# Kernel optimization log

Hardware: AMD Instinct MI355X
Metric: run time of the kernel (lower is better)

The kernel has to match this reference:

```python
import jax, jax.numpy as jnp
import numpy as np

B, N, E = 128, 300, 300        # batch, nodes (max_length), edges per sample
DIN, DH, DOUT = 768, 256, 256  # input feat, gcn hidden, gcn output
R = 26                         # NUM_DEP_TYPES
NHEADS, HDIM = 8, DH // 8


def setup_inputs() -> dict:
    key = jax.random.key(0)
    ks = jax.random.split(key, 12)
    s = lambda d: 1.0 / np.sqrt(d)
    return {
        "node_features": jax.random.normal(ks[0], (B, N, DIN), jnp.float32),
        "src": jax.random.randint(ks[1], (B, E), 0, N, jnp.int32),
        "dst": jax.random.randint(ks[2], (B, E), 0, N, jnp.int32),
        "etype": jax.random.randint(ks[3], (B, E), 0, R, jnp.int32),
        "W_rel": jax.random.normal(ks[4], (R, DIN, DH), jnp.float32) * s(DIN),
        "W_loop": jax.random.normal(ks[5], (DIN, DH), jnp.float32) * s(DIN),
        "b_rel": jnp.zeros((DH,), jnp.float32),
        "in_proj_w": jax.random.normal(ks[6], (3 * DH, DH), jnp.float32) * s(DH),
        "in_proj_b": jnp.zeros((3 * DH,), jnp.float32),
        "out_proj_w": jax.random.normal(ks[7], (DH, DH), jnp.float32) * s(DH),
        "out_proj_b": jnp.zeros((DH,), jnp.float32),
        "mlp_w": jax.random.normal(ks[8], (DOUT, DH), jnp.float32) * s(DH),
        "mlp_b": jnp.zeros((DOUT,), jnp.float32),
    }


def reference(node_features, src, dst, etype, W_rel, W_loop, b_rel,
              in_proj_w, in_proj_b, out_proj_w, out_proj_b, mlp_w, mlp_b):
    # ---- RelGraphConv (regularizer=None, self_loop=True, sum aggregation) ----
    # gather source-node features per edge: [B, E, DIN]
    h_src = jnp.take_along_axis(node_features, src[..., None].astype(jnp.int32), axis=1)
    # per-relation masked matmul: msg[b,e] = h_src[b,e] @ W_rel[etype[b,e]]
    msg = jnp.zeros((B, E, DH), node_features.dtype)
    for r in range(R):  # fixed small relation set
        mask = (etype == r)[..., None]
        msg = msg + jnp.einsum('bei,io->beo', jnp.where(mask, h_src, 0.0), W_rel[r])
    # scatter-add messages to destination nodes
    b_idx = jnp.arange(B)[:, None]
    agg = jnp.zeros((B, N, DH), node_features.dtype).at[b_idx, dst].add(msg)
    h = agg + jnp.einsum('bni,io->bno', node_features, W_loop) + b_rel  # [B, N, DH]

    # ---- MultiheadAttention (self-attn over nodes, eval mode) ----
    qkv = jnp.einsum('bnd,ed->bne', h, in_proj_w) + in_proj_b
    q, k, v = jnp.split(qkv, 3, axis=-1)
    q = q.reshape(B, N, NHEADS, HDIM)
    k = k.reshape(B, N, NHEADS, HDIM)
    v = v.reshape(B, N, NHEADS, HDIM)
    scores = jnp.einsum('bqhd,bkhd->bhqk', q, k) / np.sqrt(HDIM)
    attn = jax.nn.softmax(scores, axis=-1)
    ctx = jnp.einsum('bhqk,bkhd->bqhd', attn, v).reshape(B, N, DH)
    attn_out = jnp.einsum('bnd,ed->bne', ctx, out_proj_w) + out_proj_b

    # ---- mean-pool over nodes + MLP ----
    pooled = jnp.mean(attn_out, axis=1)  # [B, DH]
    return pooled @ mlp_w.T + mlp_b      # [B, DOUT]
```

## Files before the change

### kernel.cpp

```cpp
#include <hip/hip_runtime.h>
#include <hip/hip_bf16.h>
#include <cstdint>
#include <cstddef>

#define BB 128
#define NN 300
#define EE 300
#define DIN 768
#define DH 256
#define NREL 26
#define NHEADS 8
#define HDIM 32
#define MTOT (BB*NN)
#define NEDGE (BB*EE)
#define NHB 150

typedef __attribute__((ext_vector_type(8))) short bf16x8;
typedef __attribute__((ext_vector_type(4))) float f32x4;
typedef unsigned short u16;
union BU { uint4 u; bf16x8 v; };

__device__ __forceinline__ unsigned int packbf2(float a, float b) {
    unsigned int ua = __float_as_uint(a);
    unsigned int ub = __float_as_uint(b);
    ua = (ua + 0x7FFFu + ((ua >> 16) & 1u)) >> 16;
    ub = (ub + 0x7FFFu + ((ub >> 16) & 1u)) & 0xFFFF0000u;
    return ua | ub;
}
__device__ __forceinline__ u16 packbf1(float a) {
    unsigned int ua = __float_as_uint(a);
    return (u16)((ua + 0x7FFFu + ((ua >> 16) & 1u)) >> 16);
}
__device__ __forceinline__ unsigned cvtpk(float a, float b) {
    union { __hip_bfloat162 h; unsigned u; } cv;
    cv.h = __float22bfloat162_rn(make_float2(a, b));
    return cv.u;
}

__global__ __launch_bounds__(256) void b_hist(const int* __restrict__ etype,
                                              int* __restrict__ blockhist) {
    __shared__ int hist[NREL];
    const int tid = threadIdx.x;
    if (tid < NREL) hist[tid] = 0;
    __syncthreads();
    atomicAdd(&hist[etype[blockIdx.x * 256 + tid]], 1);
    __syncthreads();
    if (tid < NREL) blockhist[blockIdx.x * NREL + tid] = hist[tid];
}

__global__ __launch_bounds__(64) void b_scan(const int* __restrict__ blockhist,
                                             int* __restrict__ blockbase,
                                             int* __restrict__ cnt, int* __restrict__ off) {
    __shared__ int tot[NREL];
    const int r = threadIdx.x;
    if (r < NREL) {
        int run = 0;
        for (int b = 0; b < NHB; ++b) {
            blockbase[b * NREL + r] = run;
            run += blockhist[b * NREL + r];
        }
        tot[r] = run;
        cnt[r] = run;
    }
    __syncthreads();
    __shared__ int offs[NREL + 1];
    if (r == 0) {
        int acc = 0;
        for (int q = 0; q < NREL; ++q) { offs[q] = acc; off[q] = acc; acc += tot[q]; }
        offs[NREL] = acc; off[NREL] = acc;
    }
    __syncthreads();
    if (r < NREL) {
        int o = offs[r];
        for (int b = 0; b < NHB; ++b) blockbase[b * NREL + r] += o;
    }
}

__global__ __launch_bounds__(256) void b_scatter(const int* __restrict__ etype,
                                                 const int* __restrict__ blockbase,
                                                 int* __restrict__ list) {
    __shared__ int wavehist[4][NREL];
    __shared__ int waveoff[4][NREL];
    const int tid = threadIdx.x;
    const int w = tid >> 6, l = tid & 63;
    const int i = blockIdx.x * 256 + tid;
    const int r = etype[i];
    unsigned long long mymask = 0ull;
    #pragma unroll
    for (int q = 0; q < NREL; ++q) {
        unsigned long long m = __ballot(r == q);
        if (l == 0) wavehist[w][q] = __popcll(m);
        if (r == q) mymask = m;
    }
    const int myrank = __popcll(mymask & ((1ull << l) - 1ull));
    __syncthreads();
    if (tid < NREL) {
        int acc = 0;
        #pragma unroll
        for (int ww = 0; ww < 4; ++ww) { waveoff[ww][tid] = acc; acc += wavehist[ww][tid]; }
    }
    __syncthreads();
    list[blockbase[blockIdx.x * NREL + r] + waveoff[w][r] + myrank] = i;
}

__global__ __launch_bounds__(128) void z_tail(uint4* __restrict__ vg4) {
    const int p = blockIdx.x;
    const int tid = threadIdx.x;
    const int f = (tid < 64) ? 9 : 19;
    const int t = tid & 63;
    vg4[(size_t)(p * 20 + f) * 64 + t] = make_uint4(0u, 0u, 0u, 0u);
}

__global__ __launch_bounds__(256) void c_cast8(const float4* __restrict__ in,
                                               uint4* __restrict__ out, int n8) {
    int i = blockIdx.x * 256 + threadIdx.x;
    if (i < n8) {
        float4 f0 = in[2*i], f1 = in[2*i+1];
        uint4 o;
        o.x = packbf2(f0.x, f0.y); o.y = packbf2(f0.z, f0.w);
        o.z = packbf2(f1.x, f1.y); o.w = packbf2(f1.z, f1.w);
        out[i] = o;
    }
}

__global__ __launch_bounds__(256) void c_cast_w(
    const float* __restrict__ wrel, const float* __restrict__ wl, const float* __restrict__ wq,
    uint4* __restrict__ wrb, uint4* __restrict__ wlb, uint4* __restrict__ wqb) {
    int t = blockIdx.x * 256 + threadIdx.x;
    int l = t & 63, fid = t >> 6;
    if (fid < NREL*24*16) {
        int r = fid / 384, rem = fid - r * 384;
        int kf = rem >> 4, nt = rem & 15;
        int k0 = 32*kf + 8*(l >> 4), n = 16*nt + (l & 15);
        const float* p = wrel + ((size_t)r*768 + k0) * 256 + n;
        uint4 o;
        o.x = packbf2(p[0], p[256]); o.y = packbf2(p[512], p[768]);
        o.z = packbf2(p[1024], p[1280]); o.w = packbf2(p[1536], p[1792]);
        wrb[t] = o;
    } else if (fid < NREL*24*16 + 384) {
        int f2 = fid - NREL*24*16;
        int kf = f2 >> 4, nt = f2 & 15;
        int k0 = 32*kf + 8*(l >> 4), n = 16*nt + (l & 15);
        const float* p = wl + (size_t)k0 * 256 + n;
        uint4 o;
        o.x = packbf2(p[0], p[256]); o.y = packbf2(p[512], p[768]);
        o.z = packbf2(p[1024], p[1280]); o.w = packbf2(p[1536], p[1792]);
        wlb[f2*64 + l] = o;
    } else {
        int f2 = fid - NREL*24*16 - 384;
        int kf = f2 / 48, nt = f2 % 48;
        int e = 16*nt + (l & 15), d0 = 32*kf + 8*(l >> 4);
        const float4* p = (const float4*)(wq + (size_t)e * 256 + d0);
        float4 f0 = p[0], f1 = p[1];
        uint4 o;
        o.x = packbf2(f0.x, f0.y); o.y = packbf2(f0.z, f0.w);
        o.z = packbf2(f1.x, f1.y); o.w = packbf2(f1.z, f1.w);
        wqb[f2*64 + l] = o;
    }
}

__global__ __launch_bounds__(256) void k1m(
    const uint4* __restrict__ xb, const uint4* __restrict__ wlb,
    const float* __restrict__ brel, float* __restrict__ h) {
    __shared__ uint4 As[1024];
    const int tid = threadIdx.x;
    const int m0 = blockIdx.x * 128;
    const int nb = blockIdx.y;
    const int w = tid >> 6, l = tid & 63;
    const int g = l >> 4, q = l & 15;
    int cA[4];
    #pragma unroll
    for (int p = 0; p < 4; ++p) {
        int s = tid + p * 256;
        int fi = s >> 6, l2 = s & 63;
        int kf = fi >> 3, mt = fi & 7;
        int row = m0 + 16*mt + (l2 & 15);
        cA[p] = row * 96 + 4*kf + (l2 >> 4);
    }
    f32x4 acc[8][2];
    #pragma unroll
    for (int a = 0; a < 8; ++a)
        #pragma unroll
        for (int n = 0; n < 2; ++n) acc[a][n] = (f32x4){0.f,0.f,0.f,0.f};

    for (int step = 0; step < 12; ++step) {
        uint4 a0 = xb[cA[0] + step*8];
        uint4 a1 = xb[cA[1] + step*8];
        uint4 a2 = xb[cA[2] + step*8];
        uint4 a3 = xb[cA[3] + step*8];
        BU Bf[2][2];
        #pragma unroll
        for (int kf = 0; kf < 2; ++kf)
            #pragma unroll
            for (int nt = 0; nt < 2; ++nt)
                Bf[kf][nt].u = wlb[((step*2 + kf)*16 + nb*8 + w*2 + nt)*64 + l];
        __syncthreads();
        As[tid] = a0; As[tid + 256] = a1; As[tid + 512] = a2; As[tid + 768] = a3;
        __syncthreads();
        #pragma unroll
        for (int kf = 0; kf < 2; ++kf) {
            #pragma unroll
            for (int mt = 0; mt < 8; ++mt) {
                BU Af; Af.u = As[(kf*8 + mt)*64 + l];
                #pragma unroll
                for (int nt = 0; nt < 2; ++nt)
                    acc[mt][nt] = __builtin_amdgcn_mfma_f32_16x16x32_bf16(Af.v, Bf[kf][nt].v, acc[mt][nt], 0, 0, 0);
            }
        }
    }
    #pragma unroll
    for (int nt = 0; nt < 2; ++nt) {
        int col = nb*128 + w*32 + nt*16 + q;
        float bias = brel[col];
        #pragma unroll
        for (int mt = 0; mt < 8; ++mt)
            #pragma unroll
            for (int i = 0; i < 4; ++i)
                h[(size_t)(m0 + 16*mt + 4*g + i)*256 + col] = acc[mt][nt][i] + bias;
    }
}

__global__ __launch_bounds__(256) void k2m(
    const uint4* __restrict__ xb, const uint4* __restrict__ wrb,
    const int* __restrict__ src, const int* __restrict__ dst,
    const int* __restrict__ cnt, const int* __restrict__ off,
    const int* __restrict__ list, float* __restrict__ h) {
    __shared__ uint4 As[1024];
    __shared__ int arow_s[128];
    __shared__ int drow_s[128];
    const int r = blockIdx.y;
    const int c_total = cnt[r];
    const int t0 = blockIdx.x * 128;
    if (t0 >= c_total) return;
    const int nb = blockIdx.z;
    const int tid = threadIdx.x;
    if (tid < 128) {
        int e = t0 + tid;
        int ar = 0, dr = -1;
        if (e < c_total) {
            int eid = list[off[r] + e];
            int b = eid / EE;
            ar = b * NN + src[eid];
            dr = b * NN + dst[eid];
        }
        arow_s[tid] = ar; drow_s[tid] = dr;
    }
    __syncthreads();
    const int w = tid >> 6, l = tid & 63;
    const int g = l >> 4, q = l & 15;
    int cA[4];
    #pragma unroll
    for (int p = 0; p < 4; ++p) {
        int s = tid + p * 256;
        int fi = s >> 6, l2 = s & 63;
        int kf = fi >> 3, mt = fi & 7;
        int row = arow_s[16*mt + (l2 & 15)];
        cA[p] = row * 96 + 4*kf + (l2 >> 4);
    }
    const uint4* wb = wrb + (size_t)r * 24*16*64;
    f32x4 acc[8][2];
    #pragma unroll
    for (int a = 0; a < 8; ++a)
        #pragma unroll
        for (int n = 0; n < 2; ++n) acc[a][n] = (f32x4){0.f,0.f,0.f,0.f};

    for (int step = 0; step < 12; ++step) {
        uint4 a0 = xb[cA[0] + step*8];
        uint4 a1 = xb[cA[1] + step*8];
        uint4 a2 = xb[cA[2] + step*8];
        uint4 a3 = xb[cA[3] + step*8];
        BU Bf[2][2];
        #pragma unroll
        for (int kf = 0; kf < 2; ++kf)
            #pragma unroll
            for (int nt = 0; nt < 2; ++nt)
                Bf[kf][nt].u = wb[((step*2 + kf)*16 + nb*8 + w*2 + nt)*64 + l];
        __syncthreads();
        As[tid] = a0; As[tid + 256] = a1; As[tid + 512] = a2; As[tid + 768] = a3;
        __syncthreads();
        #pragma unroll
        for (int kf = 0; kf < 2; ++kf) {
            #pragma unroll
            for (int mt = 0; mt < 8; ++mt) {
                BU Af; Af.u = As[(kf*8 + mt)*64 + l];
                #pragma unroll
                for (int nt = 0; nt < 2; ++nt)
                    acc[mt][nt] = __builtin_amdgcn_mfma_f32_16x16x32_bf16(Af.v, Bf[kf][nt].v, acc[mt][nt], 0, 0, 0);
            }
        }
    }
    #pragma unroll
    for (int mt = 0; mt < 8; ++mt)
        #pragma unroll
        for (int i = 0; i < 4; ++i) {
            int dr = drow_s[16*mt + 4*g + i];
            if (dr >= 0) {
                #pragma unroll
                for (int nt = 0; nt < 2; ++nt)
                    atomicAdd(&h[(size_t)dr*256 + nb*128 + w*32 + nt*16 + q], acc[mt][nt][i]);
            }
        }
}

__global__ __launch_bounds__(256) void k3m(
    const float* __restrict__ h, const uint4* __restrict__ wqb,
    const float* __restrict__ bq,
    u16* __restrict__ qg, u16* __restrict__ kg, u16* __restrict__ vg) {
    __shared__ uint4 Aall[2048];
    const int tid = threadIdx.x;
    const int m0 = blockIdx.x * 64;
    const int w = tid >> 6, l = tid & 63;
    const int g = l >> 4, q = l & 15;

    #pragma unroll
    for (int p = 0; p < 8; ++p) {
        int s = tid + p * 256;
        int fi = s >> 6, l2 = s & 63;
        int kf = fi >> 2, mt = fi & 3;
        int row = m0 + 16*mt + (l2 & 15);
        int k0 = 32*kf + 8*(l2 >> 4);
        const float4* hp = (const float4*)(h + (size_t)row * 256 + k0);
        float4 f0 = hp[0], f1 = hp[1];
        uint4 o;
        o.x = packbf2(f0.x, f0.y); o.y = packbf2(f0.z, f0.w);
        o.z = packbf2(f1.x, f1.y); o.w = packbf2(f1.z, f1.w);
        Aall[s] = o;
    }
    __syncthreads();

    for (int nb = 0; nb < 6; ++nb) {
        f32x4 acc[4][2];
        #pragma unroll
        for (int a = 0; a < 4; ++a)
            #pragma unroll
            for (int n = 0; n < 2; ++n) acc[a][n] = (f32x4){0.f,0.f,0.f,0.f};

        #pragma unroll
        for (int step = 0; step < 4; ++step) {
            BU Bf[2][2];
            #pragma unroll
            for (int kf = 0; kf < 2; ++kf)
                #pragma unroll
                for (int nt = 0; nt < 2; ++nt)
                    Bf[kf][nt].u = wqb[((step*2 + kf)*48 + nb*8 + w*2 + nt)*64 + l];
            #pragma unroll
            for (int kf = 0; kf < 2; ++kf) {
                #pragma unroll
                for (int mt = 0; mt < 4; ++mt) {
                    BU Af; Af.u = Aall[((step*2 + kf)*4 + mt)*64 + l];
                    #pragma unroll
                    for (int nt = 0; nt < 2; ++nt)
                        acc[mt][nt] = __builtin_amdgcn_mfma_f32_16x16x32_bf16(Af.v, Bf[kf][nt].v, acc[mt][nt], 0, 0, 0);
                }
            }
        }
        #pragma unroll
        for (int nt = 0; nt < 2; ++nt) {
            int e = nb*128 + w*32 + nt*16 + q;
            float bias = bq[e];
            int region = e >> 8;
            int hh = (e & 255) >> 5;
            int d  = e & 31;
            u16* outb = (region == 0) ? qg : (region == 1) ? kg : vg;
            #pragma unroll
            for (int mt = 0; mt < 4; ++mt) {
                #pragma unroll
                for (int i = 0; i < 4; ++i) {
                    int j = m0 + 16*mt + 4*g + i;
                    int b_ = j / 300;
                    int jn = j - b_ * 300;
                    u16 val = packbf1(acc[mt][nt][i] + bias);
                    size_t byte;
                    if (region < 2) {
                        int word = ((b_*8 + hh)*19 + (jn >> 4))*64 + 16*(d >> 3) + (jn & 15);
                        byte = (size_t)word*16 + (size_t)(d & 7)*2;
                    } else {
                        int word = ((b_*8 + hh)*20 + (d >> 4)*10 + (jn >> 5))*64 + 16*((jn >> 3) & 3) + (d & 15);
                        byte = (size_t)word*16 + (size_t)(jn & 7)*2;
                    }
                    *(u16*)((char*)outb + byte) = val;
                }
            }
        }
    }
}

__global__ __launch_bounds__(256) void k4_attn(
    const uint4* __restrict__ qg, const uint4* __restrict__ kg,
    const uint4* __restrict__ vg, float* __restrict__ pooled) {
    __shared__ uint4 kf_s[19*64];
    __shared__ uint4 vt_s[20*64];
    __shared__ __align__(16) u16 pbuf[4][2560];
    __shared__ float pool_lds[4][32];
    const int bh = blockIdx.x;
    const int tid = threadIdx.x;
    for (int s = tid; s < 19*64; s += 256) kf_s[s] = kg[(size_t)bh*19*64 + s];
    for (int s = tid; s < 20*64; s += 256) vt_s[s] = vg[(size_t)bh*20*64 + s];
    __syncthreads();

    const int w = tid >> 6, l = tid & 63;
    const int g = l >> 4, q = l & 15;
    char* pwbase = (char*)pbuf[w] + 256*(g >> 1) + 16*q + 8*(g & 1);
    const uint4* prd = (const uint4*)pbuf[w];

    const float c1 = 0.17677669529663687f * 1.4426950408889634f;
    float pool[8] = {0.f,0.f,0.f,0.f,0.f,0.f,0.f,0.f};

    for (int qt = w; qt < 19; qt += 4) {
        const int qrow = qt * 16 + q;
        BU uq; uq.u = qg[(size_t)(bh*19 + qt)*64 + l];
        float lsum = 0.f;
        f32x4 ctx0 = {0.f,0.f,0.f,0.f}, ctx1 = {0.f,0.f,0.f,0.f};

        #pragma unroll
        for (int half = 0; half < 2; ++half) {
            #pragma unroll
            for (int jj = 0; jj < 10; ++jj) {
                const int jt = half*10 + jj;
                uint2 pk = make_uint2(0u, 0u);
                if (jt < 19) {
                    BU uk; uk.u = kf_s[jt*64 + l];
                    f32x4 z = {0.f,0.f,0.f,0.f};
                    f32x4 s4 = __builtin_amdgcn_mfma_f32_16x16x32_bf16(uk.v, uq.v, z, 0, 0, 0);
                    float p0 = exp2f(s4[0]*c1);
                    float p1 = exp2f(s4[1]*c1);
                    float p2 = exp2f(s4[2]*c1);
                    float p3 = exp2f(s4[3]*c1);
                    if (jt == 18 && g == 3) { p0 = 0.f; p1 = 0.f; p2 = 0.f; p3 = 0.f; }
                    lsum += (p0 + p1) + (p2 + p3);
                    pk.x = cvtpk(p0, p1);
                    pk.y = cvtpk(p2, p3);
                }
                *(uint2*)(pwbase + 512*jj) = pk;
            }
            #pragma unroll
            for (int cc = 0; cc < 5; ++cc) {
                const int cg = half*5 + cc;
                BU up;  up.u  = prd[cc*64 + l];
                BU uv0; uv0.u = vt_s[cg*64 + l];
                BU uv1; uv1.u = vt_s[(10 + cg)*64 + l];
                ctx0 = __builtin_amdgcn_mfma_f32_16x16x32_bf16(uv0.v, up.v, ctx0, 0, 0, 0);
                ctx1 = __builtin_amdgcn_mfma_f32_16x16x32_bf16(uv1.v, up.v, ctx1, 0, 0, 0);
            }
        }
        lsum += __shfl_xor(lsum, 16);
        lsum += __shfl_xor(lsum, 32);
        if (qrow < NN) {
            float inv = 1.0f / lsum;
            pool[0] += ctx0[0] * inv; pool[1] += ctx0[1] * inv;
            pool[2] += ctx0[2] * inv; pool[3] += ctx0[3] * inv;
            pool[4] += ctx1[0] * inv; pool[5] += ctx1[1] * inv;
            pool[6] += ctx1[2] * inv; pool[7] += ctx1[3] * inv;
        }
    }

    #pragma unroll
    for (int i = 0; i < 8; ++i) {
        float v = pool[i];
        v += __shfl_xor(v, 1); v += __shfl_xor(v, 2);
        v += __shfl_xor(v, 4); v += __shfl_xor(v, 8);
        pool[i] = v;
    }
    if (q == 0) {
        #pragma unroll
        for (int dt = 0; dt < 2; ++dt)
            #pragma unroll
            for (int i = 0; i < 4; ++i)
                pool_lds[w][dt * 16 + 4 * g + i] = pool[dt * 4 + i];
    }
    __syncthreads();
    if (tid < 32) {
        int b = bh >> 3, hh = bh & 7;
        float s = pool_lds[0][tid] + pool_lds[1][tid] + pool_lds[2][tid] + pool_lds[3][tid];
        pooled[(size_t)b * DH + hh * HDIM + tid] = s * (1.0f / 300.0f);
    }
}

__global__ __launch_bounds__(256) void k5_head(
    const float* __restrict__ pooled, const float* __restrict__ wo, const float* __restrict__ bo,
    const float* __restrict__ wm, const float* __restrict__ bm, float* __restrict__ out) {
    __shared__ float pc[DH];
    __shared__ float t1[DH];
    const int b = blockIdx.x, tid = threadIdx.x;
    pc[tid] = pooled[(size_t)b * DH + tid];
    __syncthreads();
    float acc = bo[tid];
    for (int d = 0; d < DH; ++d) acc += pc[d] * wo[(size_t)tid * DH + d];
    t1[tid] = acc;
    __syncthreads();
    float acc2 = bm[tid];
    for (int e2 = 0; e2 < DH; ++e2) acc2 += t1[e2] * wm[(size_t)tid * DH + e2];
    out[(size_t)b * DH + tid] = acc2;
}

extern "C" void kernel_launch(void* const* d_in, const int* in_sizes, int n_in,
                              void* d_out, int out_size, void* d_ws, size_t ws_size,
                              hipStream_t stream) {
    (void)in_sizes; (void)n_in; (void)out_size; (void)ws_size;
    const float* x     = (const float*)d_in[0];
    const int*   src   = (const int*)d_in[1];
    const int*   dst   = (const int*)d_in[2];
    const int*   etype = (const int*)d_in[3];
    const float* wrel  = (const float*)d_in[4];
    const float* wloop = (const float*)d_in[5];
    const float* brel  = (const float*)d_in[6];
    const float* wq    = (const float*)d_in[7];
    const float* bq    = (const float*)d_in[8];
    const float* wo    = (const float*)d_in[9];
    const float* bo    = (const float*)d_in[10];
    const float* wm    = (const float*)d_in[11];
    const float* bm    = (const float*)d_in[12];
    float* out = (float*)d_out;

    char* W = (char*)d_ws;
    float* h      = (float*)W;
    u16*   vg     = (u16*)W;
    u16*   xb     = (u16*)(W + 39321600ull);
    u16*   qg     = xb;
    u16*   kg     = (u16*)(W + 39321600ull + 19922944ull);
    u16*   hb_dead= (u16*)(W + 39321600ull + 58982400ull);
    uint4* wrb    = (uint4*)(W + 39321600ull + 58982400ull + 19660800ull);
    uint4* wlb    = (uint4*)((char*)wrb + 10223616ull);
    uint4* wqb    = (uint4*)((char*)wlb + 393216ull);
    float* pooled = (float*)((char*)wqb + 393216ull);
    int*   ibase  = (int*)((char*)pooled + 131072ull);
    int*   cnt    = ibase;
    int*   off    = ibase + 32;
    int*   list   = ibase + 64;
    int*   blockhist = list + NEDGE;
    int*   blockbase = blockhist + NHB*NREL;
    (void)hb_dead;

    vg = (u16*)((char*)(blockbase + NHB*NREL) + 256);
    vg = (u16*)(((uintptr_t)vg + 255) & ~(uintptr_t)255);

    b_hist<<<NHB, 256, 0, stream>>>(etype, blockhist);
    b_scan<<<1, 64, 0, stream>>>(blockhist, blockbase, cnt, off);
    b_scatter<<<NHB, 256, 0, stream>>>(etype, blockbase, list);

    c_cast8<<<14400, 256, 0, stream>>>((const float4*)x, (uint4*)xb, 3686400);
    c_cast_w<<<2688, 256, 0, stream>>>(wrel, wloop, wq, wrb, wlb, wqb);

    k1m<<<dim3(300, 2), 256, 0, stream>>>((const uint4*)xb, wlb, brel, h);
    k2m<<<dim3(16, 26, 2), 256, 0, stream>>>((const uint4*)xb, wrb, src, dst, cnt, off, list, h);
    z_tail<<<1024, 128, 0, stream>>>((uint4*)vg);
    k3m<<<600, 256, 0, stream>>>(h, wqb, bq, qg, kg, vg);
    k4_attn<<<BB * NHEADS, 256, 0, stream>>>((const uint4*)qg, (const uint4*)kg, (const uint4*)vg, pooled);
    k5_head<<<BB, 256, 0, stream>>>(pooled, wo, bo, wm, bm, out);
}
```

Measured before the change: 285.0 us.

## Pre-cast h to bf16 and split QKV projection across output blocks in grid

Adds a separate cast kernel that converts the fp32 GCN output h to bf16 once. The QKV projection kernel now launches one block per (64-row tile, 128-column output block), giving 3600 blocks instead of 600, and streams the bf16 A tile through a small LDS buffer per k-step instead of staging the full 64x256 tile. This raises parallelism and lowers LDS use per block. The cost is an extra kernel launch and an extra pass over h, and each A tile is now read six times from global memory or cache.

```diff
diff --git a/kernel.cpp b/kernel.cpp
--- a/kernel.cpp
+++ b/kernel.cpp
@@ -303,83 +303,79 @@
 }
 
 __global__ __launch_bounds__(256) void k3m(
-    const float* __restrict__ h, const uint4* __restrict__ wqb,
+    const uint4* __restrict__ hb, const uint4* __restrict__ wqb,
     const float* __restrict__ bq,
     u16* __restrict__ qg, u16* __restrict__ kg, u16* __restrict__ vg) {
-    __shared__ uint4 Aall[2048];
+    __shared__ uint4 As[512];
     const int tid = threadIdx.x;
     const int m0 = blockIdx.x * 64;
+    const int nb = blockIdx.y;
     const int w = tid >> 6, l = tid & 63;
     const int g = l >> 4, q = l & 15;
-
-    #pragma unroll
-    for (int p = 0; p < 8; ++p) {
+    int cA[2];
+    #pragma unroll
+    for (int p = 0; p < 2; ++p) {
         int s = tid + p * 256;
         int fi = s >> 6, l2 = s & 63;
         int kf = fi >> 2, mt = fi & 3;
         int row = m0 + 16*mt + (l2 & 15);
-        int k0 = 32*kf + 8*(l2 >> 4);
-        const float4* hp = (const float4*)(h + (size_t)row * 256 + k0);
-        float4 f0 = hp[0], f1 = hp[1];
-        uint4 o;
-        o.x = packbf2(f0.x, f0.y); o.y = packbf2(f0.z, f0.w);
-        o.z = packbf2(f1.x, f1.y); o.w = packbf2(f1.z, f1.w);
-        Aall[s] = o;
-    }
-    __syncthreads();
-
-    for (int nb = 0; nb < 6; ++nb) {
-        f32x4 acc[4][2];
-        #pragma unroll
-        for (int a = 0; a < 4; ++a)
-            #pragma unroll
-            for (int n = 0; n < 2; ++n) acc[a][n] = (f32x4){0.f,0.f,0.f,0.f};
-
-        #pragma unroll
-        for (int step = 0; step < 4; ++step) {
-            BU Bf[2][2];
-            #pragma unroll
-            for (int kf = 0; kf < 2; ++kf)
+        cA[p] = row * 32 + 4*kf + (l2 >> 4);
+    }
+    f32x4 acc[4][2];
+    #pragma unroll
+    for (int a = 0; a < 4; ++a)
+        #pragma unroll
+        for (int n = 0; n < 2; ++n) acc[a][n] = (f32x4){0.f,0.f,0.f,0.f};
+
+    for (int step = 0; step < 4; ++step) {
+        uint4 a0 = hb[cA[0] + step*8];
+        uint4 a1 = hb[cA[1] + step*8];
+        BU Bf[2][2];
+        #pragma unroll
+        for (int kf = 0; kf < 2; ++kf)
+            #pragma unroll
+            for (int nt = 0; nt < 2; ++nt)
+                Bf[kf][nt].u = wqb[((step*2 + kf)*48 + nb*8 + w*2 + nt)*64 + l];
+        __syncthreads();
+        As[tid] = a0; As[tid + 256] = a1;
+        __syncthreads();
+        #pragma unroll
+        for (int kf = 0; kf < 2; ++kf) {
+            BU Af[4];
+            #pragma unroll
+            for (int mt = 0; mt < 4; ++mt) Af[mt].u = As[(kf*4 + mt)*64 + l];
+            #pragma unroll
+            for (int mt = 0; mt < 4; ++mt)
                 #pragma unroll
                 for (int nt = 0; nt < 2; ++nt)
-                    Bf[kf][nt].u = wqb[((step*2 + kf)*48 + nb*8 + w*2 + nt)*64 + l];
-            #pragma unroll
-            for (int kf = 0; kf < 2; ++kf) {
-                #pragma unroll
-                for (int mt = 0; mt < 4; ++mt) {
-                    BU Af; Af.u = Aall[((step*2 + kf)*4 + mt)*64 + l];
-                    #pragma unroll
-                    for (int nt = 0; nt < 2; ++nt)
-                        acc[mt][nt] = __builtin_amdgcn_mfma_f32_16x16x32_bf16(Af.v, Bf[kf][nt].v, acc[mt][nt], 0, 0, 0);
+                    acc[mt][nt] = __builtin_amdgcn_mfma_f32_16x16x32_bf16(Af[mt].v, Bf[kf][nt].v, acc[mt][nt], 0, 0, 0);
+        }
+    }
+    #pragma unroll
+    for (int nt = 0; nt < 2; ++nt) {
+        int e = nb*128 + w*32 + nt*16 + q;
+        float bias = bq[e];
+        int region = e >> 8;
+        int hh = (e & 255) >> 5;
+        int d  = e & 31;
+        u16* outb = (region == 0) ? qg : (region == 1) ? kg : vg;
+        #pragma unroll
+        for (int mt = 0; mt < 4; ++mt) {
+            #pragma unroll
+            for (int i = 0; i < 4; ++i) {
+                int j = m0 + 16*mt + 4*g + i;
+                int b_ = j / 300;
+                int jn = j - b_ * 300;
+                u16 val = packbf1(acc[mt][nt][i] + bias);
+                size_t byte;
+                if (region < 2) {
+                    int word = ((b_*8 + hh)*19 + (jn >> 4))*64 + 16*(d >> 3) + (jn & 15);
+                    byte = (size_t)word*16 + (size_t)(d & 7)*2;
+                } else {
+                    int word = ((b_*8 + hh)*20 + (d >> 4)*10 + (jn >> 5))*64 + 16*((jn >> 3) & 3) + (d & 15);
+                    byte = (size_t)word*16 + (size_t)(jn & 7)*2;
                 }
-            }
-        }
-        #pragma unroll
-        for (int nt = 0; nt < 2; ++nt) {
-            int e = nb*128 + w*32 + nt*16 + q;
-            float bias = bq[e];
-            int region = e >> 8;
-            int hh = (e & 255) >> 5;
-            int d  = e & 31;
-            u16* outb = (region == 0) ? qg : (region == 1) ? kg : vg;
-            #pragma unroll
-            for (int mt = 0; mt < 4; ++mt) {
-                #pragma unroll
-                for (int i = 0; i < 4; ++i) {
-                    int j = m0 + 16*mt + 4*g + i;
-                    int b_ = j / 300;
-                    int jn = j - b_ * 300;
-                    u16 val = packbf1(acc[mt][nt][i] + bias);
-                    size_t byte;
-                    if (region < 2) {
-                        int word = ((b_*8 + hh)*19 + (jn >> 4))*64 + 16*(d >> 3) + (jn & 15);
-                        byte = (size_t)word*16 + (size_t)(d & 7)*2;
-                    } else {
-                        int word = ((b_*8 + hh)*20 + (d >> 4)*10 + (jn >> 5))*64 + 16*((jn >> 3) & 3) + (d & 15);
-                        byte = (size_t)word*16 + (size_t)(jn & 7)*2;
-                    }
-                    *(u16*)((char*)outb + byte) = val;
-                }
+                *(u16*)((char*)outb + byte) = val;
             }
         }
     }
@@ -514,11 +510,10 @@
 
     char* W = (char*)d_ws;
     float* h      = (float*)W;
-    u16*   vg     = (u16*)W;
     u16*   xb     = (u16*)(W + 39321600ull);
     u16*   qg     = xb;
     u16*   kg     = (u16*)(W + 39321600ull + 19922944ull);
-    u16*   hb_dead= (u16*)(W + 39321600ull + 58982400ull);
+    u16*   hb     = (u16*)(W + 39321600ull + 58982400ull);
     uint4* wrb    = (uint4*)(W + 39321600ull + 58982400ull + 19660800ull);
     uint4* wlb    = (uint4*)((char*)wrb + 10223616ull);
     uint4* wqb    = (uint4*)((char*)wlb + 393216ull);
@@ -529,9 +524,7 @@
     int*   list   = ibase + 64;
     int*   blockhist = list + NEDGE;
     int*   blockbase = blockhist + NHB*NREL;
-    (void)hb_dead;
-
-    vg = (u16*)((char*)(blockbase + NHB*NREL) + 256);
+    u16*   vg = (u16*)((char*)(blockbase + NHB*NREL) + 256);
     vg = (u16*)(((uintptr_t)vg + 255) & ~(uintptr_t)255);
 
     b_hist<<<NHB, 256, 0, stream>>>(etype, blockhist);
@@ -543,8 +536,9 @@
 
     k1m<<<dim3(300, 2), 256, 0, stream>>>((const uint4*)xb, wlb, brel, h);
     k2m<<<dim3(16, 26, 2), 256, 0, stream>>>((const uint4*)xb, wrb, src, dst, cnt, off, list, h);
+    c_cast8<<<4800, 256, 0, stream>>>((const float4*)h, (uint4*)hb, 1228800);
     z_tail<<<1024, 128, 0, stream>>>((uint4*)vg);
-    k3m<<<600, 256, 0, stream>>>(h, wqb, bq, qg, kg, vg);
+    k3m<<<dim3(600, 6), 256, 0, stream>>>((const uint4*)hb, wqb, bq, qg, kg, vg);
     k4_attn<<<BB * NHEADS, 256, 0, stream>>>((const uint4*)qg, (const uint4*)kg, (const uint4*)vg, pooled);
     k5_head<<<BB, 256, 0, stream>>>(pooled, wo, bo, wm, bm, out);
 }
```

Result: faster. 276.7 us (-2.9%).
